# Kernel optimization log

Hardware: AMD Instinct MI355X
Metric: run time of the kernel (lower is better)

Reference implementation:

```python
import jax, jax.numpy as jnp
import numpy as np
import math

DIMS = 2560
N_HEADS = 32
ROT_DIM = 32  # partial rotary (Phi-2)
BASE = 10000.0
B, L = 1, 2048


def apply_rope(x, rot_dim=ROT_DIM, base=BASE, offset=0):
    # x: [B, H, L, hd]; rotate first rot_dim features, pass rest through
    Lx = x.shape[2]
    D = rot_dim // 2
    pos = jnp.arange(offset, offset + Lx, dtype=jnp.float32)              # [L]
    freq = jnp.exp(-jnp.arange(D, dtype=jnp.float32) * (math.log(base) / D))  # [D]
    theta = pos[:, None] * freq[None, :]                                   # [L, D]
    cos, sin = jnp.cos(theta), jnp.sin(theta)
    x1 = x[..., :D]
    x2 = x[..., D:rot_dim]
    rx1 = x1 * cos - x2 * sin
    rx2 = x1 * sin + x2 * cos
    return jnp.concatenate([rx1, rx2, x[..., rot_dim:]], axis=-1)


def setup_inputs() -> dict:
    key = jax.random.key(0)
    k1, k2, k3, k4, k5 = jax.random.split(key, 5)
    x = jax.random.normal(k1, (B, L, DIMS), dtype=jnp.float32)
    Wqkv_w = jax.random.normal(k2, (3 * DIMS, DIMS), dtype=jnp.float32) * 0.02
    Wqkv_b = jax.random.normal(k3, (3 * DIMS,), dtype=jnp.float32) * 0.02
    out_w = jax.random.normal(k4, (DIMS, DIMS), dtype=jnp.float32) * 0.02
    out_b = jax.random.normal(k5, (DIMS,), dtype=jnp.float32) * 0.02
    # additive causal mask, broadcast over batch/heads
    mask = jnp.triu(jnp.full((L, L), -1e9, dtype=jnp.float32), k=1)[None, None]
    return {"x": x, "Wqkv_w": Wqkv_w, "Wqkv_b": Wqkv_b,
            "out_w": out_w, "out_b": out_b, "mask": mask}


def reference(x, Wqkv_w, Wqkv_b, out_w, out_b, mask):
    Bx, Lx, _ = x.shape
    hd = DIMS // N_HEADS  # 80
    qkv = x @ Wqkv_w.T + Wqkv_b                          # [B, L, 3*dims]
    q, k, v = jnp.split(qkv, 3, axis=-1)
    def to_heads(t):
        return t.reshape(Bx, Lx, N_HEADS, hd).transpose(0, 2, 1, 3)  # [B,H,L,hd]
    q, k, v = to_heads(q), to_heads(k), to_heads(v)
    q = apply_rope(q)
    k = apply_rope(k)
    scale = 1.0 / math.sqrt(hd)
    scores = scale * jnp.einsum('bhqd,bhkd->bhqk', q, k) + mask  # [B,H,L,L]
    probs = jax.nn.softmax(scores, axis=-1)
    out = jnp.einsum('bhqk,bhkd->bhqd', probs, v)
    out = out.transpose(0, 2, 1, 3).reshape(Bx, Lx, DIMS)
    return out @ out_w.T + out_b
```

## Files before the change

kernel.cpp:

```cpp
#include <hip/hip_runtime.h>
#include <cstdint>
#include <cmath>

typedef __attribute__((ext_vector_type(4))) float f32x4;
typedef __attribute__((ext_vector_type(8))) short s16x8;

#define LOG2E 1.4426950408889634f

__device__ __forceinline__ unsigned short f2bf(float f) {
    unsigned int u = __float_as_uint(f);
    u += 0x7FFFu + ((u >> 16) & 1u);
    return (unsigned short)(u >> 16);
}
__device__ __forceinline__ float bf2f(unsigned short s) {
    return __uint_as_float(((unsigned int)s) << 16);
}

__device__ __forceinline__ void async_copy16(const void* g, void* l) {
    __builtin_amdgcn_global_load_lds(
        (const __attribute__((address_space(1))) unsigned int*)(uintptr_t)g,
        (__attribute__((address_space(3))) unsigned int*)(uintptr_t)l,
        16, 0, 0);
}

__global__ __launch_bounds__(256) void cast_bf16_kernel(const float* __restrict__ in,
                                                        unsigned short* __restrict__ out,
                                                        int n4) {
    int i = blockIdx.x * 256 + threadIdx.x;
    if (i < n4) {
        float4 v = ((const float4*)in)[i];
        ushort4 o;
        o.x = f2bf(v.x); o.y = f2bf(v.y); o.z = f2bf(v.z); o.w = f2bf(v.w);
        ((ushort4*)out)[i] = o;
    }
}

template <bool BF16_OUT, bool ATOMIC>
__global__ __launch_bounds__(256) void gemm_bt(const unsigned short* __restrict__ A,
                                               const unsigned short* __restrict__ B,
                                               const float* __restrict__ bias,
                                               void* __restrict__ Cout,
                                               int M, int N, int K) {
    __shared__ unsigned short As[128 * 32];
    __shared__ unsigned short Bs[128 * 32];
    const int tid  = threadIdx.x;
    const int lane = tid & 63;
    const int wv   = tid >> 6;
    const int m0 = blockIdx.y * 128;
    const int n0 = blockIdx.x * 128;
    const int w_row = (wv >> 1) * 64;
    const int w_col = (wv & 1) * 64;
    const int fr = lane & 15;
    const int fg = lane >> 4;
    const int srow = lane >> 2;
    const int scol = (((lane & 3) ^ ((lane >> 3) & 3)) * 8);
    const int rofs = ((fg ^ ((fr >> 1) & 3)) * 8);
    const int c0 = wv * 2;

    int kstart = 0, kend = K;
    if (ATOMIC) {
        kstart = blockIdx.z * (K >> 1);
        kend   = kstart + (K >> 1);
    }

    f32x4 acc[4][4];
    const f32x4 zf = {0.f, 0.f, 0.f, 0.f};
    for (int r = 0; r < 4; ++r)
        for (int c = 0; c < 4; ++c) acc[r][c] = zf;

    for (int k0 = kstart; k0 < kend; k0 += 32) {
        for (int c = c0; c < c0 + 2; ++c) {
            const unsigned short* gA = A + (size_t)(m0 + c * 16 + srow) * K + (k0 + scol);
            async_copy16(gA, &As[c * 512]);
            const unsigned short* gB = B + (size_t)(n0 + c * 16 + srow) * K + (k0 + scol);
            async_copy16(gB, &Bs[c * 512]);
        }
        __syncthreads();
        s16x8 af[4], bf[4];
        for (int r = 0; r < 4; ++r)
            af[r] = *(const s16x8*)&As[(w_row + r * 16 + fr) * 32 + rofs];
        for (int c = 0; c < 4; ++c)
            bf[c] = *(const s16x8*)&Bs[(w_col + c * 16 + fr) * 32 + rofs];
        for (int r = 0; r < 4; ++r)
            for (int c = 0; c < 4; ++c)
                acc[r][c] = __builtin_amdgcn_mfma_f32_16x16x32_bf16(af[r], bf[c], acc[r][c], 0, 0, 0);
        __syncthreads();
    }

    const int rb = (lane >> 4) * 4;
    const bool addb = !ATOMIC || blockIdx.z == 0;
    for (int c = 0; c < 4; ++c) {
        int col = n0 + w_col + c * 16 + fr;
        float bv = addb ? bias[col] : 0.f;
        for (int r = 0; r < 4; ++r) {
            int row = m0 + w_row + r * 16 + rb;
            for (int q = 0; q < 4; ++q) {
                float v = acc[r][c][q] + bv;
                if constexpr (ATOMIC) {
                    unsafeAtomicAdd(&((float*)Cout)[(size_t)(row + q) * N + col], v);
                } else if constexpr (BF16_OUT) {
                    ((unsigned short*)Cout)[(size_t)(row + q) * N + col] = f2bf(v);
                } else {
                    ((float*)Cout)[(size_t)(row + q) * N + col] = v;
                }
            }
        }
    }
}

__global__ __launch_bounds__(256) void rope_q_kernel(unsigned short* __restrict__ qkv) {
    int g = blockIdx.x * 256 + threadIdx.x;
    int c = g & 1;
    int h = (g >> 1) & 31;
    int p = g >> 6;
    size_t base = (size_t)p * 7680 + h * 80 + c * 8;
    s16x8 x1v = *(const s16x8*)(qkv + base);
    s16x8 x2v = *(const s16x8*)(qkv + base + 16);
    s16x8 o1, o2;
    for (int j = 0; j < 8; ++j) {
        int dp = c * 8 + j;
        float freq = expf(-(float)dp * 0.57564627324851142f);
        float sn, cs;
        sincosf((float)p * freq, &sn, &cs);
        float x1 = bf2f((unsigned short)x1v[j]);
        float x2 = bf2f((unsigned short)x2v[j]);
        o1[j] = (short)f2bf(x1 * cs - x2 * sn);
        o2[j] = (short)f2bf(x1 * sn + x2 * cs);
    }
    *(s16x8*)(qkv + base)      = o1;
    *(s16x8*)(qkv + base + 16) = o2;
}

__global__ __launch_bounds__(256) void rope_pack_k_kernel(const unsigned short* __restrict__ qkv,
                                                          unsigned short* __restrict__ Kp) {
    int g = blockIdx.x * 256 + threadIdx.x;
    int c   = g % 12;
    int h   = (g / 12) & 31;
    int pos = g / 384;
    int d0 = c * 8;
    const unsigned short* kb = qkv + (size_t)pos * 7680 + 2560 + h * 80;
    s16x8 v = {0, 0, 0, 0, 0, 0, 0, 0};
    if (c >= 4) {
        if (d0 < 80) v = *(const s16x8*)(kb + d0);
    } else if (c < 2) {
        s16x8 x1v = *(const s16x8*)(kb + d0);
        s16x8 x2v = *(const s16x8*)(kb + d0 + 16);
        for (int j = 0; j < 8; ++j) {
            int dp = d0 + j;
            float freq = expf(-(float)dp * 0.57564627324851142f);
            float sn, cs;
            sincosf((float)pos * freq, &sn, &cs);
            v[j] = (short)f2bf(bf2f((unsigned short)x1v[j]) * cs -
                               bf2f((unsigned short)x2v[j]) * sn);
        }
    } else {
        s16x8 x1v = *(const s16x8*)(kb + d0 - 16);
        s16x8 x2v = *(const s16x8*)(kb + d0);
        for (int j = 0; j < 8; ++j) {
            int dp = d0 - 16 + j;
            float freq = expf(-(float)dp * 0.57564627324851142f);
            float sn, cs;
            sincosf((float)pos * freq, &sn, &cs);
            v[j] = (short)f2bf(bf2f((unsigned short)x1v[j]) * sn +
                               bf2f((unsigned short)x2v[j]) * cs);
        }
    }
    *(s16x8*)(Kp + ((size_t)h * 2048 + pos) * 96 + d0) = v;
}

__global__ __launch_bounds__(256) void pack_v_kernel(const unsigned short* __restrict__ qkv,
                                                     unsigned short* __restrict__ Vp) {
    int h  = blockIdx.x & 31;
    int g64 = blockIdx.x >> 5;
    int k0 = g64 * 64;
    int tid = threadIdx.x;
    for (int ci = tid; ci < 320; ci += 256) {
        int d   = ci % 80;
        int kbl = ci / 80;
        unsigned short tmp[16];
        for (int j = 0; j < 16; ++j)
            tmp[j] = qkv[(size_t)(k0 + kbl * 16 + j) * 7680 + 5120 + h * 80 + d];
        unsigned short* dst = Vp + ((size_t)h * 128 + g64 * 4 + kbl) * 1280 + d * 16;
        *(s16x8*)dst       = *(const s16x8*)&tmp[0];
        *(s16x8*)(dst + 8) = *(const s16x8*)&tmp[8];
    }
}

__global__ __launch_bounds__(256) void flash3_kernel(const unsigned short* __restrict__ qkv,
                                                     const unsigned short* __restrict__ Kp,
                                                     const unsigned short* __restrict__ Vp,
                                                     unsigned short* __restrict__ attn) {
    __shared__ unsigned short Pt[4][640];
    __shared__ float parts[2][16][84];
    __shared__ float parts_l[2][16];
    const int tid  = threadIdx.x;
    const int lane = tid & 63;
    const int wv   = tid >> 6;
    const int h = blockIdx.x & 31;
    const int p = blockIdx.x >> 5;
    const int s    = (wv < 2) ? p : (127 - p);
    const int j    = wv & 1;
    const int slot = wv >> 1;
    const int fr = lane & 15;
    const int fg = lane >> 4;
    const float k1 = 0.11180339887498949f * LOG2E;
    const int sm16 = s * 16;

    const int n    = s + 1;
    const int half = (n + 1) >> 1;
    const int kstart = (j ? half : 0) * 16;
    const int kend   = (j ? n : half) * 16;

    s16x8 qf[3];
    {
        const unsigned short* qb = qkv + (size_t)(sm16 + fr) * 7680 + h * 80;
        const s16x8 zs = {0, 0, 0, 0, 0, 0, 0, 0};
        for (int sd = 0; sd < 3; ++sd) {
            int d = 32 * sd + fg * 8;
            qf[sd] = (d < 80) ? *(const s16x8*)(qb + d) : zs;
        }
    }

    f32x4 O[5];
    const f32x4 zf = {0.f, 0.f, 0.f, 0.f};
    for (int t = 0; t < 5; ++t) O[t] = zf;
    float rs[4] = {0.f, 0.f, 0.f, 0.f};

    const unsigned short* kptr = Kp + (size_t)h * 2048 * 96 + (size_t)(kstart + fr) * 96 + fg * 8;
    const unsigned short* vptr = Vp + (size_t)h * 128 * 1280 + (size_t)(kstart >> 4) * 1280
                                 + (fg >> 1) * 1280 + fr * 16 + (fg & 1) * 8;
    unsigned short* Pw = &Pt[wv][0];

    for (int k0 = kstart; k0 < kend; k0 += 32) {
        s16x8 kb[2][3];
        for (int g = 0; g < 2; ++g)
            for (int sd = 0; sd < 3; ++sd)
                kb[g][sd] = *(const s16x8*)(kptr + g * 1536 + sd * 32);
        s16x8 vb[5];
        for (int t = 0; t < 5; ++t)
            vb[t] = *(const s16x8*)(vptr + t * 256);

        f32x4 sa[2] = {zf, zf};
        for (int g = 0; g < 2; ++g)
            for (int sd = 0; sd < 3; ++sd)
                sa[g] = __builtin_amdgcn_mfma_f32_16x16x32_bf16(qf[sd], kb[g][sd], sa[g], 0, 0, 0);

        if (k0 + 32 > sm16 || k0 + 32 > kend) {
            for (int g = 0; g < 2; ++g)
                for (int r = 0; r < 4; ++r) {
                    int key  = k0 + g * 16 + fr;
                    int qrow = sm16 + fg * 4 + r;
                    if (key > qrow || key >= kend) sa[g][r] = -1e30f;
                }
        }

        float pr[2][4];
        for (int g = 0; g < 2; ++g)
            for (int r = 0; r < 4; ++r)
                pr[g][r] = __builtin_amdgcn_exp2f(sa[g][r] * k1);
        for (int r = 0; r < 4; ++r) rs[r] += pr[0][r] + pr[1][r];
        for (int g = 0; g < 2; ++g)
            for (int r = 0; r < 4; ++r)
                Pw[(fg * 4 + r) * 40 + g * 16 + fr] =
                    (unsigned short)(__float_as_uint(pr[g][r]) >> 16);

        s16x8 pa = *(const s16x8*)(Pw + fr * 40 + fg * 8);
        for (int t = 0; t < 5; ++t)
            O[t] = __builtin_amdgcn_mfma_f32_16x16x32_bf16(pa, vb[t], O[t], 0, 0, 0);

        kptr += 3072;
        vptr += 2560;
    }

    for (int r = 0; r < 4; ++r) {
        float v = rs[r];
        v += __shfl_xor(v, 1);
        v += __shfl_xor(v, 2);
        v += __shfl_xor(v, 4);
        v += __shfl_xor(v, 8);
        rs[r] = v;
    }

    if (j) {
        for (int t = 0; t < 5; ++t)
            for (int r = 0; r < 4; ++r)
                parts[slot][fg * 4 + r][t * 16 + fr] = O[t][r];
        if (fr == 0)
            for (int r = 0; r < 4; ++r) parts_l[slot][fg * 4 + r] = rs[r];
    }
    __syncthreads();
    if (!j) {
        for (int r = 0; r < 4; ++r) {
            float rl = 1.0f / (rs[r] + parts_l[slot][fg * 4 + r]);
            int row = sm16 + fg * 4 + r;
            for (int t = 0; t < 5; ++t) {
                float v = (O[t][r] + parts[slot][fg * 4 + r][t * 16 + fr]) * rl;
                attn[(size_t)row * 2560 + h * 80 + t * 16 + fr] = f2bf(v);
            }
        }
    }
}

extern "C" void kernel_launch(void* const* d_in, const int* in_sizes, int n_in,
                              void* d_out, int out_size, void* d_ws, size_t ws_size,
                              hipStream_t stream) {
    const float* x    = (const float*)d_in[0];
    const float* wqkv = (const float*)d_in[1];
    const float* bqkv = (const float*)d_in[2];
    const float* outw = (const float*)d_in[3];
    const float* outb = (const float*)d_in[4];

    unsigned short* xb    = (unsigned short*)d_ws;
    unsigned short* wqkvb = xb + (size_t)2048 * 2560;
    unsigned short* Kp    = wqkvb;
    unsigned short* Vp    = wqkvb + (size_t)32 * 2048 * 96;
    unsigned short* outwb = wqkvb + (size_t)7680 * 2560;
    unsigned short* qkvb  = outwb + (size_t)2560 * 2560;
    unsigned short* attnb = qkvb  + (size_t)2048 * 7680;
    float* out = (float*)d_out;

    cast_bf16_kernel<<<2048 * 2560 / 4 / 256, 256, 0, stream>>>(x, xb, 2048 * 2560 / 4);
    cast_bf16_kernel<<<7680 * 2560 / 4 / 256, 256, 0, stream>>>(wqkv, wqkvb, 7680 * 2560 / 4);
    cast_bf16_kernel<<<2560 * 2560 / 4 / 256, 256, 0, stream>>>(outw, outwb, 2560 * 2560 / 4);

    gemm_bt<true, false><<<dim3(7680 / 128, 2048 / 128), 256, 0, stream>>>(
        xb, wqkvb, bqkv, (void*)qkvb, 2048, 7680, 2560);

    rope_q_kernel<<<2048 * 64 / 256, 256, 0, stream>>>(qkvb);
    rope_pack_k_kernel<<<2048 * 384 / 256, 256, 0, stream>>>(qkvb, Kp);
    pack_v_kernel<<<32 * 32, 256, 0, stream>>>(qkvb, Vp);

    flash3_kernel<<<2048, 256, 0, stream>>>(qkvb, Kp, Vp, attnb);

    hipMemsetAsync(d_out, 0, (size_t)2048 * 2560 * 4, stream);
    gemm_bt<false, true><<<dim3(2560 / 128, 2048 / 128, 2), 256, 0, stream>>>(
        attnb, outwb, outb, (void*)out, 2048, 2560, 2560);
}
```

Measured before the change: 492.2 us.

## Double GEMM K-tile to 64 and drop split-K atomics for output projection

The GEMM now stages 64-wide K slices in LDS with a new XOR swizzle and runs two MFMA sub-steps per barrier pair, which halves the number of synchronisations per unit of work. The output projection no longer uses split-K with atomic adds and a preceding memset. It now launches a plain 320-block grid that writes results directly. This removes the atomic traffic and the memset, but the output GEMM has fewer blocks to fill the GPU, and the larger LDS tile may reduce occupancy.

```diff
diff --git a/kernel.cpp b/kernel.cpp
--- a/kernel.cpp
+++ b/kernel.cpp
@@ -35,14 +35,14 @@
     }
 }
 
-template <bool BF16_OUT, bool ATOMIC>
+template <bool BF16_OUT>
 __global__ __launch_bounds__(256) void gemm_bt(const unsigned short* __restrict__ A,
                                                const unsigned short* __restrict__ B,
                                                const float* __restrict__ bias,
                                                void* __restrict__ Cout,
                                                int M, int N, int K) {
-    __shared__ unsigned short As[128 * 32];
-    __shared__ unsigned short Bs[128 * 32];
+    __shared__ unsigned short As[128 * 64];
+    __shared__ unsigned short Bs[128 * 64];
     const int tid  = threadIdx.x;
     const int lane = tid & 63;
     const int wv   = tid >> 6;
@@ -52,57 +52,61 @@
     const int w_col = (wv & 1) * 64;
     const int fr = lane & 15;
     const int fg = lane >> 4;
-    const int srow = lane >> 2;
-    const int scol = (((lane & 3) ^ ((lane >> 3) & 3)) * 8);
-    const int rofs = ((fg ^ ((fr >> 1) & 3)) * 8);
-    const int c0 = wv * 2;
-
-    int kstart = 0, kend = K;
-    if (ATOMIC) {
-        kstart = blockIdx.z * (K >> 1);
-        kend   = kstart + (K >> 1);
-    }
+    const int srow = lane >> 3;
+    const int scol = ((lane & 7) ^ srow) * 8;
+    const int rofs0 = ((fg ^ (fr & 7))) * 8;
+    const int rofs1 = rofs0 ^ 32;
 
     f32x4 acc[4][4];
     const f32x4 zf = {0.f, 0.f, 0.f, 0.f};
     for (int r = 0; r < 4; ++r)
         for (int c = 0; c < 4; ++c) acc[r][c] = zf;
 
-    for (int k0 = kstart; k0 < kend; k0 += 32) {
-        for (int c = c0; c < c0 + 2; ++c) {
-            const unsigned short* gA = A + (size_t)(m0 + c * 16 + srow) * K + (k0 + scol);
-            async_copy16(gA, &As[c * 512]);
-            const unsigned short* gB = B + (size_t)(n0 + c * 16 + srow) * K + (k0 + scol);
-            async_copy16(gB, &Bs[c * 512]);
-        }
+    const unsigned short* gA = A + (size_t)(m0 + wv * 32 + srow) * K + scol;
+    const unsigned short* gB = B + (size_t)(n0 + wv * 32 + srow) * K + scol;
+    const int ldsbase = (wv * 32 + srow) * 64;
+
+    for (int k0 = 0; k0 < K; k0 += 64) {
+        for (int i = 0; i < 4; ++i)
+            async_copy16(gA + (size_t)i * 8 * K + k0, &As[(wv * 32 + i * 8) * 64]);
+        for (int i = 0; i < 4; ++i)
+            async_copy16(gB + (size_t)i * 8 * K + k0, &Bs[(wv * 32 + i * 8) * 64]);
         __syncthreads();
-        s16x8 af[4], bf[4];
-        for (int r = 0; r < 4; ++r)
-            af[r] = *(const s16x8*)&As[(w_row + r * 16 + fr) * 32 + rofs];
-        for (int c = 0; c < 4; ++c)
-            bf[c] = *(const s16x8*)&Bs[(w_col + c * 16 + fr) * 32 + rofs];
-        for (int r = 0; r < 4; ++r)
+        {
+            s16x8 af[4], bf[4];
+            for (int r = 0; r < 4; ++r)
+                af[r] = *(const s16x8*)&As[(w_row + r * 16 + fr) * 64 + rofs0];
             for (int c = 0; c < 4; ++c)
-                acc[r][c] = __builtin_amdgcn_mfma_f32_16x16x32_bf16(af[r], bf[c], acc[r][c], 0, 0, 0);
+                bf[c] = *(const s16x8*)&Bs[(w_col + c * 16 + fr) * 64 + rofs0];
+            for (int r = 0; r < 4; ++r)
+                for (int c = 0; c < 4; ++c)
+                    acc[r][c] = __builtin_amdgcn_mfma_f32_16x16x32_bf16(af[r], bf[c], acc[r][c], 0, 0, 0);
+        }
+        {
+            s16x8 af[4], bf[4];
+            for (int r = 0; r < 4; ++r)
+                af[r] = *(const s16x8*)&As[(w_row + r * 16 + fr) * 64 + rofs1];
+            for (int c = 0; c < 4; ++c)
+                bf[c] = *(const s16x8*)&Bs[(w_col + c * 16 + fr) * 64 + rofs1];
+            for (int r = 0; r < 4; ++r)
+                for (int c = 0; c < 4; ++c)
+                    acc[r][c] = __builtin_amdgcn_mfma_f32_16x16x32_bf16(af[r], bf[c], acc[r][c], 0, 0, 0);
+        }
         __syncthreads();
     }
 
     const int rb = (lane >> 4) * 4;
-    const bool addb = !ATOMIC || blockIdx.z == 0;
     for (int c = 0; c < 4; ++c) {
         int col = n0 + w_col + c * 16 + fr;
-        float bv = addb ? bias[col] : 0.f;
+        float bv = bias[col];
         for (int r = 0; r < 4; ++r) {
             int row = m0 + w_row + r * 16 + rb;
             for (int q = 0; q < 4; ++q) {
                 float v = acc[r][c][q] + bv;
-                if constexpr (ATOMIC) {
-                    unsafeAtomicAdd(&((float*)Cout)[(size_t)(row + q) * N + col], v);
-                } else if constexpr (BF16_OUT) {
+                if constexpr (BF16_OUT)
                     ((unsigned short*)Cout)[(size_t)(row + q) * N + col] = f2bf(v);
-                } else {
+                else
                     ((float*)Cout)[(size_t)(row + q) * N + col] = v;
-                }
             }
         }
     }
@@ -323,7 +327,7 @@
     cast_bf16_kernel<<<7680 * 2560 / 4 / 256, 256, 0, stream>>>(wqkv, wqkvb, 7680 * 2560 / 4);
     cast_bf16_kernel<<<2560 * 2560 / 4 / 256, 256, 0, stream>>>(outw, outwb, 2560 * 2560 / 4);
 
-    gemm_bt<true, false><<<dim3(7680 / 128, 2048 / 128), 256, 0, stream>>>(
+    gemm_bt<true><<<dim3(7680 / 128, 2048 / 128), 256, 0, stream>>>(
         xb, wqkvb, bqkv, (void*)qkvb, 2048, 7680, 2560);
 
     rope_q_kernel<<<2048 * 64 / 256, 256, 0, stream>>>(qkvb);
@@ -332,7 +336,6 @@
 
     flash3_kernel<<<2048, 256, 0, stream>>>(qkvb, Kp, Vp, attnb);
 
-    hipMemsetAsync(d_out, 0, (size_t)2048 * 2560 * 4, stream);
-    gemm_bt<false, true><<<dim3(2560 / 128, 2048 / 128, 2), 256, 0, stream>>>(
+    gemm_bt<false><<<dim3(2560 / 128, 2048 / 128), 256, 0, stream>>>(
         attnb, outwb, outb, (void*)out, 2048, 2560, 2560);
 }
```

Result: faster. 442.3 us (-10.1%).
